# Optimization experiments

Measured on AMD Instinct MI355X. Metric: run time of the kernel, lower is better.

## Reference

```python
import jax, jax.numpy as jnp
import numpy as np

B, T, N, P, L = 8, 96, 20000, 12, 3
D = 32          # d_model (forced by channel-count identity d_model+96 == 4*d_model)
C = 4 * D       # 128 channels inside the linearized conv layers
M = 64          # random_feature_dim
TAU = 0.25
EPS = 1e-6      # numerical_stabilizer in random_feature_map


def _proj_matrix(m, d, seed=0):
    # create_random_matrix: stacked transposed-Q blocks from QR of gaussian blocks,
    # scaled row-wise by norms of a gaussian matrix (scaling=0).
    rng = np.random.RandomState(seed)
    blocks = []
    n_full = m // d
    for _ in range(n_full):
        q, _ = np.linalg.qr(rng.randn(d, d))
        blocks.append(q.T)
    rem = m - n_full * d
    if rem:
        q, _ = np.linalg.qr(rng.randn(d, d))
        blocks.append(q.T[:rem])
    mat = np.vstack(blocks)
    mult = np.linalg.norm(rng.randn(m, d), axis=1)
    return jnp.asarray(mult[:, None] * mat, dtype=jnp.float32)


def setup_inputs() -> dict:
    key = jax.random.key(0)
    ks = jax.random.split(key, 12)
    g = lambda k, shape, s=0.05: jax.random.normal(k, shape, jnp.float32) * s
    return {
        "x": jax.random.normal(ks[0], (B, T, N), jnp.float32),
        "x_mark": jax.random.uniform(ks[1], (B, T, 2), dtype=jnp.float32),
        "node_emb": g(ks[2], (N, D), 0.1),
        "time_tab": g(ks[3], (T, D), 0.1),
        "week_tab": g(ks[4], (7, D), 0.1),
        "input_w": g(ks[5], (D, 3 * T)),
        "input_b": jnp.zeros((D,), jnp.float32),
        "w1_w": g(ks[6], (D, 3 * D)),
        "w1_b": jnp.zeros((D,), jnp.float32),
        "w2_w": g(ks[7], (D, 3 * D)),
        "w2_b": jnp.zeros((D,), jnp.float32),
        "in_w": g(ks[8], (L, C, C)),
        "in_b": jnp.zeros((L, C), jnp.float32),
        "out_w": g(ks[9], (L, C, C)),
        "out_b": jnp.zeros((L, C), jnp.float32),
        "ln_g": jnp.ones((L, C), jnp.float32),
        "ln_b": jnp.zeros((L, C), jnp.float32),
        "reg_w": g(ks[10], (P, 2 * C)),
        "reg_b": jnp.zeros((P,), jnp.float32),
        "proj": _proj_matrix(M, D, seed=0),
    }


def _rfm(data, proj, is_query):
    # FAVOR+ positive random features (head dim == 1 folded out; shapes are [B,N,d])
    d = data.shape[-1]
    data = data * (float(d) ** -0.25)            # h(x) normalizer d^{-1/4}
    ratio = 1.0 / np.sqrt(float(proj.shape[0]))
    dash = jnp.einsum('bnd,md->bnm', data, proj)
    diag = 0.5 * jnp.sum(data * data, axis=-1, keepdims=True)
    if is_query:
        stab = jnp.max(dash, axis=-1, keepdims=True)          # per-row max
    else:
        stab = jnp.max(dash, axis=(1, 2), keepdims=True)      # max over features AND nodes
    return ratio * (jnp.exp(dash - diag - stab) + EPS)


def _linear_kernel(v, phi_q, phi_k):
    # associativity trick: (phi_q (phi_k^T v)) / (phi_q (phi_k^T 1))
    kv = jnp.einsum('bnm,bnc->bmc', phi_k, v)
    num = jnp.einsum('bnm,bmc->bnc', phi_q, kv)
    den = jnp.einsum('bnm,bm->bn', phi_q, jnp.sum(phi_k, axis=1))
    return num / den[..., None]


def reference(x, x_mark, node_emb, time_tab, week_tab, input_w, input_b,
              w1_w, w1_b, w2_w, w2_b, in_w, in_b, out_w, out_b,
              ln_g, ln_b, reg_w, reg_b, proj):
    Bq, Tq, Nq = x.shape
    marks = jax.lax.stop_gradient(x_mark)
    tod_idx = jnp.clip((marks[:, -1, 0] * Tq).astype(jnp.int32), 0, Tq - 1)
    dow_idx = jnp.clip((marks[:, -1, 1] * 7.0).astype(jnp.int32), 0, 6)
    time_e = jnp.broadcast_to(time_tab[tod_idx][:, None, :], (Bq, Nq, D))
    week_e = jnp.broadcast_to(week_tab[dow_idx][:, None, :], (Bq, Nq, D))
    node_e = jnp.broadcast_to(node_emb[None], (Bq, Nq, D))

    # input embedding over the flattened (feature-major) [3*T] channel axis
    tod_f = jnp.broadcast_to(x_mark[:, :, 0:1], (Bq, Tq, Nq))
    dow_f = jnp.broadcast_to(x_mark[:, :, 1:2], (Bq, Tq, Nq))
    feat = jnp.concatenate([x, tod_f, dow_f], axis=1)          # (B, 3T, N)
    x_in = jnp.einsum('bkn,ck->bnc', feat, input_w) + input_b  # (B, N, D)

    xg = jnp.concatenate([node_e, time_e, week_e], axis=-1)        # (B,N,3D)
    h = jnp.concatenate([x_in, node_e, time_e, week_e], axis=-1)   # (B,N,4D)

    inv_sqrt_tau = 1.0 / np.sqrt(TAU)
    nv1 = (jnp.einsum('bng,cg->bnc', xg, w1_w) + w1_b) * inv_sqrt_tau
    nv2 = (jnp.einsum('bng,cg->bnc', xg, w2_w) + w2_b) * inv_sqrt_tau
    # same node vectors (hence same data-derived seed / projection) every layer
    phi_q = _rfm(nv1, proj, True)    # (B,N,M)
    phi_k = _rfm(nv2, proj, False)   # (B,N,M)

    skip = h
    for i in range(L):
        res = h
        u = jax.nn.sigmoid(h @ in_w[i].T + in_b[i]) * (h @ out_w[i].T + out_b[i])
        u = _linear_kernel(u, phi_q, phi_k)
        h = u + res
        mu = jnp.mean(h, axis=-1, keepdims=True)
        var = jnp.var(h, axis=-1, keepdims=True)
        h = (h - mu) * jax.lax.rsqrt(var + 1e-5) * ln_g[i] + ln_b[i]

    out = jnp.concatenate([skip, h], axis=-1) @ reg_w.T + reg_b  # (B,N,P)
    return jnp.swapaxes(out, 1, 2)                               # (B,P,N)
```

## Files before the change

### kernel.cpp

```cpp
#include <hip/hip_runtime.h>

typedef unsigned short u16;
typedef __attribute__((ext_vector_type(8))) __bf16 bf16x8;
typedef __attribute__((ext_vector_type(4))) float f32x4;

#define BB 8
#define TT 96
#define NN 20000
#define NP 20160
#define PP 12
#define LL 3
#define DD 32
#define CC 128
#define MM 64
#define NB3 105
#define NB5 313

constexpr float KSC  = 0.8408964152537145f;
constexpr float KSC2 = 0.7071067811865476f;

__device__ inline u16 f2bf(float f){
  unsigned u = __float_as_uint(f);
  u = (u + 0x7fffu + ((u >> 16) & 1u)) >> 16;
  return (u16)u;
}
__device__ inline float bf2f(u16 h){ return __uint_as_float(((unsigned)h) << 16); }
__device__ inline unsigned fmapu(float f){
  unsigned u = __float_as_uint(f);
  return (u & 0x80000000u) ? ~u : (u | 0x80000000u);
}
__device__ inline float funmap(unsigned u){
  return (u & 0x80000000u) ? __uint_as_float(u & 0x7fffffffu) : __uint_as_float(~u);
}
__device__ inline unsigned pk2(float a, float b){
  return (unsigned)f2bf(a) | ((unsigned)f2bf(b) << 16);
}

__global__ void k0_prep(const float* xm, const float* time_tab, const float* week_tab,
                        const float* w1w, const float* w1b, const float* w2w, const float* w2b,
                        const float* inw, const float* inb, const float* proj,
                        float* bv1, float* bv2, float* sbd1, float* sbd2,
                        float* bc1, float* bc2, float* mb, int* tod, int* dow,
                        unsigned* cmx, float* ksum)
{
  __shared__ float sT[BB][DD], sWk[BB][DD];
  __shared__ float sB1[BB][DD], sB2[BB][DD];
  __shared__ int sTod[BB], sDow[BB];
  int tid = threadIdx.x;
  ksum[tid] = 0.f;
  if (tid < BB){
    float t0 = xm[(tid*TT + TT-1)*2 + 0];
    float t1 = xm[(tid*TT + TT-1)*2 + 1];
    int ti = (int)(t0 * (float)TT); ti = min(max(ti, 0), TT-1);
    int di = (int)(t1 * 7.0f);      di = min(max(di, 0), 6);
    sTod[tid] = ti; sDow[tid] = di; tod[tid] = ti; dow[tid] = di;
  }
  if (tid < MM) cmx[tid] = fmapu(-3e38f);
  __syncthreads();
  if (tid < BB*DD){
    int b = tid >> 5, g = tid & 31;
    sT[b][g]  = time_tab[sTod[b]*DD + g];
    sWk[b][g] = week_tab[sDow[b]*DD + g];
  }
  __syncthreads();
  {
    int which = tid >> 8, b = (tid >> 5) & 7, c = tid & 31;
    const float* w  = which ? w2w : w1w;
    const float* wb = which ? w2b : w1b;
    float s = wb[c];
    for (int g = 0; g < DD; g++)
      s += sT[b][g]*w[c*96 + 32 + g] + sWk[b][g]*w[c*96 + 64 + g];
    if (which){ bv2[b*DD+c] = s; sB2[b][c] = s; }
    else      { bv1[b*DD+c] = s; sB1[b][c] = s; }
  }
  __syncthreads();
  {
    int b = tid >> 6, m = tid & 63;
    float s1 = 0.f, s2 = 0.f;
    for (int c = 0; c < DD; c++){
      float p = proj[m*DD + c];
      s1 += sB1[b][c]*p; s2 += sB2[b][c]*p;
    }
    sbd1[b*MM+m] = KSC * s1;
    sbd2[b*MM+m] = KSC * s2;
  }
  if (tid < 16){
    int b = tid & 7;
    float s = 0.f;
    if (tid >> 3){ for (int c = 0; c < DD; c++) s += sB2[b][c]*sB2[b][c]; bc2[b] = 0.5f*KSC2*s; }
    else         { for (int c = 0; c < DD; c++) s += sB1[b][c]*sB1[b][c]; bc1[b] = 0.5f*KSC2*s; }
  }
  if (tid < 256){
    int b = tid >> 5, c = tid & 31;
    float s = inb[c];
    for (int t = 0; t < TT; t++){
      float m0 = xm[(b*TT+t)*2+0], m1 = xm[(b*TT+t)*2+1];
      s += m0 * inw[c*288 + 96 + t] + m1 * inw[c*288 + 192 + t];
    }
    mb[b*DD+c] = s;
  }
}

__global__ __launch_bounds__(256) void k1_node(
    const float* node_emb, const float* w1w, const float* w2w, const float* proj,
    const float* bv1, const float* bv2,
    const float* gin_w, const float* gout_w,
    float* sd1, float* sd2, float* sq1, float* sq2,
    float* cr1, float* cr2, unsigned* cmx,
    u16* wbf, float* kvz)
{
  __shared__ float sW1[DD][DD], sW2[DD][DD], sP[MM][DD];
  __shared__ float sB1[BB][DD], sB2[BB][DD];
  __shared__ unsigned sCM[MM];
  int tid = threadIdx.x;
  int gid = blockIdx.x*256 + tid;
  for (int i = gid; i < LL*BB*MM*CC; i += 79*256) kvz[i] = 0.f;
  for (int i = gid; i < 2*LL*CC*CC; i += 79*256){
    int which = i / (LL*CC*CC);
    int r = i - which*(LL*CC*CC);
    wbf[i] = f2bf((which ? gout_w : gin_w)[r]);
  }
  for (int i = tid; i < DD*DD; i += 256){
    int c = i >> 5, g = i & 31;
    sW1[c][g] = w1w[c*96 + g];
    sW2[c][g] = w2w[c*96 + g];
  }
  for (int i = tid; i < MM*DD; i += 256) sP[i >> 5][i & 31] = proj[i];
  if (tid < BB*DD){
    int b = tid >> 5, c = tid & 31;
    sB1[b][c] = bv1[tid]; sB2[b][c] = bv2[tid];
  }
  if (tid < MM) sCM[tid] = fmapu(-3e38f);
  __syncthreads();
  int n = blockIdx.x*256 + tid;
  bool valid = n < NN;
  int nc = valid ? n : 0;
  float nd[DD];
  #pragma unroll
  for (int g = 0; g < DD; g += 4){
    float4 v = *(const float4*)&node_emb[nc*DD + g];
    nd[g] = v.x; nd[g+1] = v.y; nd[g+2] = v.z; nd[g+3] = v.w;
  }
  float r1[DD], r2[DD];
  #pragma unroll
  for (int c = 0; c < DD; c++){ r1[c] = 0.f; r2[c] = 0.f; }
  #pragma unroll
  for (int g = 0; g < DD; g++){
    float x = nd[g];
    #pragma unroll
    for (int c = 0; c < DD; c++){ r1[c] += x*sW1[c][g]; r2[c] += x*sW2[c][g]; }
  }
  float q1 = 0.f, q2 = 0.f;
  #pragma unroll
  for (int c = 0; c < DD; c++){ q1 += r1[c]*r1[c]; q2 += r2[c]*r2[c]; }
  if (valid){ sq1[n] = 0.5f*KSC2*q1; sq2[n] = 0.5f*KSC2*q2; }
  for (int b = 0; b < BB; b++){
    float c1 = 0.f, c2 = 0.f;
    #pragma unroll
    for (int c = 0; c < DD; c++){ c1 += r1[c]*sB1[b][c]; c2 += r2[c]*sB2[b][c]; }
    if (valid){ cr1[b*NN + n] = KSC2*c1; cr2[b*NN + n] = KSC2*c2; }
  }
  for (int m = 0; m < MM; m++){
    float s1 = 0.f, s2 = 0.f;
    #pragma unroll
    for (int c = 0; c < DD; c++){ float p = sP[m][c]; s1 += r1[c]*p; s2 += r2[c]*p; }
    s1 *= KSC; s2 *= KSC;
    if (valid){
      sd1[(size_t)n*MM + m] = s1;
      sd2[(size_t)n*MM + m] = s2;
      atomicMax(&sCM[m], fmapu(s2));
    }
  }
  __syncthreads();
  if (tid < MM) atomicMax(&cmx[tid], sCM[tid]);
}

__global__ void k0b_stab(const unsigned* cmx, const float* sbd2, float* stab){
  int lane = threadIdx.x;
  float cm = funmap(cmx[lane]);
  for (int b = 0; b < BB; b++){
    float v = cm + sbd2[b*MM + lane];
    #pragma unroll
    for (int off = 32; off; off >>= 1) v = fmaxf(v, __shfl_xor(v, off));
    if (lane == 0) stab[b] = v;
  }
}

__global__ __launch_bounds__(256) void k1b_phi(
    const float* sd1, const float* sd2, const float* sq1, const float* sq2,
    const float* cr1, const float* cr2, const float* sbd1, const float* sbd2,
    const float* bc1, const float* bc2, const float* stab,
    u16* phiq, u16* phikt, float* ksum)
{
  __shared__ u16 sT[MM][264];
  __shared__ float sQb[MM], sKb[MM];
  __shared__ float sRed[256];
  int tid = threadIdx.x;
  int b = blockIdx.y, n0 = blockIdx.x*256;
  if (tid < MM){
    sQb[tid] = sbd1[b*MM + tid];
    sKb[tid] = sbd2[b*MM + tid] - bc2[b] - stab[b];
  }
  __syncthreads();
  int n = n0 + tid;
  bool v = n < NN;
  int nc = v ? n : 0;
  float dq[MM];
  const float* s1r = sd1 + (size_t)nc*MM;
  #pragma unroll
  for (int m = 0; m < MM; m += 4){
    float4 t = *(const float4*)&s1r[m];
    dq[m]=t.x; dq[m+1]=t.y; dq[m+2]=t.z; dq[m+3]=t.w;
  }
  float rm = -3e38f;
  #pragma unroll
  for (int m = 0; m < MM; m++) rm = fmaxf(rm, dq[m] + sQb[m]);
  float diagq = sq1[nc] + cr1[b*NN + nc] + bc1[b];
  u16* pqr = phiq + ((size_t)(b*NN) + nc)*MM;
  #pragma unroll
  for (int m = 0; m < MM; m += 8){
    float p[8];
    #pragma unroll
    for (int j = 0; j < 8; j++){
      float ev = dq[m+j] + sQb[m+j] - rm - diagq;
      p[j] = 0.125f*__expf(ev) + 1.25e-7f;
    }
    uint4 w = { pk2(p[0],p[1]), pk2(p[2],p[3]), pk2(p[4],p[5]), pk2(p[6],p[7]) };
    if (v) *(uint4*)&pqr[m] = w;
  }
  const float* s2r = sd2 + (size_t)nc*MM;
  float diagk = sq2[nc] + cr2[b*NN + nc];
  #pragma unroll
  for (int m = 0; m < MM; m++){
    float ev = s2r[m] + sKb[m] - diagk;
    float pv = v ? (0.125f*__expf(ev) + 1.25e-7f) : 0.f;
    sT[m][tid] = f2bf(pv);
  }
  __syncthreads();
  {
    int m = tid >> 2, q = tid & 3;
    float s = 0.f;
    for (int j = 0; j < 64; j++) s += bf2f(sT[m][q*64 + j]);
    sRed[tid] = s;
  }
  __syncthreads();
  if (tid < MM){
    float s = sRed[tid*4] + sRed[tid*4+1] + sRed[tid*4+2] + sRed[tid*4+3];
    atomicAdd(&ksum[b*MM + tid], s);
  }
  {
    int m = tid >> 2, q = tid & 3;
    int nb = n0 + q*64;
    if (nb + 64 <= NP){
      u16* dst = phikt + (size_t)(b*MM + m)*NP + nb;
      #pragma unroll
      for (int j = 0; j < 64; j += 8)
        *(uint4*)&dst[j] = *(const uint4*)&sT[m][q*64 + j];
    }
  }
}

__global__ __launch_bounds__(256) void k2_embed(
    const float* x, const float* node_emb, const float* time_tab, const float* week_tab,
    const float* inw, const float* mb, const int* tod, const int* dow,
    u16* skip)
{
  __shared__ float sWt[TT*DD];
  __shared__ float sMB[DD], sTE[DD], sWE[DD];
  int tid = threadIdx.x;
  int b = blockIdx.y;
  for (int i = tid; i < TT*DD; i += 256){
    int t = i >> 5, c = i & 31;
    sWt[i] = inw[c*288 + t];
  }
  if (tid < DD){
    sMB[tid] = mb[b*DD + tid];
    sTE[tid] = time_tab[tod[b]*DD + tid];
    sWE[tid] = week_tab[dow[b]*DD + tid];
  }
  __syncthreads();
  int n = blockIdx.x*256 + tid;
  bool valid = n < NN;
  int nc = valid ? n : 0;
  float acc[DD];
  #pragma unroll
  for (int c = 0; c < DD; c++) acc[c] = sMB[c];
  const float* xb = x + (size_t)b*TT*NN + nc;
  for (int t = 0; t < TT; t++){
    float xv = xb[(size_t)t*NN];
    #pragma unroll
    for (int c = 0; c < DD; c++) acc[c] += xv * sWt[t*DD + c];
  }
  if (!valid) return;
  float nodev[DD];
  #pragma unroll
  for (int g = 0; g < DD; g += 4){
    float4 v = *(const float4*)&node_emb[n*DD + g];
    nodev[g] = v.x; nodev[g+1] = v.y; nodev[g+2] = v.z; nodev[g+3] = v.w;
  }
  auto chv = [&](int c)->float{
    if (c < 32)  return acc[c];
    if (c < 64)  return nodev[c-32];
    if (c < 96)  return sTE[c-64];
    return sWE[c-96];
  };
  u16* dst = skip + (size_t)(b*NN + n)*CC;
  #pragma unroll
  for (int g = 0; g < CC; g += 8){
    uint4 w;
    w.x = pk2(chv(g+0), chv(g+1));
    w.y = pk2(chv(g+2), chv(g+3));
    w.z = pk2(chv(g+4), chv(g+5));
    w.w = pk2(chv(g+6), chv(g+7));
    *(uint4*)&dst[g] = w;
  }
}

__global__ __launch_bounds__(256,2) void k3_gate(
    const u16* hin, const u16* wbf, const float* inb, const float* outb,
    const u16* phikt, float* kv, int layer)
{
  __shared__ u16 sUT[CC*72];
  __shared__ float s_inb[CC], s_outb[CC];
  int tid = threadIdx.x;
  int b = blockIdx.y, blk = blockIdx.x;
  int lane = tid & 63, wave = tid >> 6, quad = lane >> 4, l15 = lane & 15;
  if (tid < CC){ s_inb[tid] = inb[layer*CC + tid]; s_outb[tid] = outb[layer*CC + tid]; }

  bf16x8 bw[4][4];
  #pragma unroll
  for (int nt = 0; nt < 4; nt++){
    int which = nt >> 1;
    int co = wave*32 + (nt & 1)*16 + l15;
    const u16* wp = wbf + ((size_t)(which*LL + layer)*CC + co)*CC;
    #pragma unroll
    for (int ks = 0; ks < 4; ks++)
      bw[ks][nt] = *(const bf16x8*)&wp[ks*32 + quad*8];
  }
  f32x4 kvacc[4][2] = {};
  const u16* hbase = hin + (size_t)(b*NN)*CC;

  for (int ch = 0; ch < 3; ch++){
    int n0 = blk*192 + ch*64;
    f32x4 acc[4][4] = {};
    bf16x8 af[2][4];
    #pragma unroll
    for (int mt = 0; mt < 4; mt++)
      af[0][mt] = *(const bf16x8*)&hbase[(size_t)(n0 + mt*16 + l15)*CC + quad*8];
    #pragma unroll
    for (int ks = 0; ks < 4; ks++){
      int cur = ks & 1, nxt = cur ^ 1;
      if (ks < 3){
        #pragma unroll
        for (int mt = 0; mt < 4; mt++)
          af[nxt][mt] = *(const bf16x8*)&hbase[(size_t)(n0 + mt*16 + l15)*CC + (ks+1)*32 + quad*8];
      }
      #pragma unroll
      for (int mt = 0; mt < 4; mt++)
        #pragma unroll
        for (int nt = 0; nt < 4; nt++)
          acc[mt][nt] = __builtin_amdgcn_mfma_f32_16x16x32_bf16(af[cur][mt], bw[ks][nt], acc[mt][nt], 0, 0, 0);
    }
    __syncthreads();
    #pragma unroll
    for (int mt = 0; mt < 4; mt++){
      int r0 = mt*16 + quad*4;
      #pragma unroll
      for (int nt = 0; nt < 2; nt++){
        int co = wave*32 + nt*16 + l15;
        float bi = s_inb[co], bo = s_outb[co];
        float uv[4];
        #pragma unroll
        for (int e = 0; e < 4; e++){
          float up = acc[mt][nt][e] + bi;
          float vp = acc[mt][nt+2][e] + bo;
          float u = vp / (1.f + __expf(-up));
          if (n0 + r0 + e >= NN) u = 0.f;
          uv[e] = u;
        }
        ushort4 hv4;
        hv4.x = f2bf(uv[0]); hv4.y = f2bf(uv[1]); hv4.z = f2bf(uv[2]); hv4.w = f2bf(uv[3]);
        *(ushort4*)&sUT[co*72 + r0] = hv4;
      }
    }
    __syncthreads();
    #pragma unroll
    for (int ks2 = 0; ks2 < 2; ks2++){
      bf16x8 ap[4], bu[2];
      #pragma unroll
      for (int mtp = 0; mtp < 4; mtp++)
        ap[mtp] = *(const bf16x8*)&phikt[(size_t)(b*MM + mtp*16 + l15)*NP + n0 + ks2*32 + quad*8];
      #pragma unroll
      for (int nt2 = 0; nt2 < 2; nt2++)
        bu[nt2] = *(const bf16x8*)&sUT[(wave*32 + nt2*16 + l15)*72 + ks2*32 + quad*8];
      #pragma unroll
      for (int mtp = 0; mtp < 4; mtp++)
        #pragma unroll
        for (int nt2 = 0; nt2 < 2; nt2++)
          kvacc[mtp][nt2] = __builtin_amdgcn_mfma_f32_16x16x32_bf16(ap[mtp], bu[nt2], kvacc[mtp][nt2], 0, 0, 0);
    }
  }
  float* kvb = kv + (size_t)(layer*BB + b)*MM*CC;
  #pragma unroll
  for (int mt = 0; mt < 4; mt++)
    #pragma unroll
    for (int nt2 = 0; nt2 < 2; nt2++)
      #pragma unroll
      for (int e = 0; e < 4; e++)
        atomicAdd(&kvb[(mt*16 + quad*4 + e)*CC + wave*32 + nt2*16 + l15], kvacc[mt][nt2][e]);
}

__global__ void k4_reduce(const float* kv, const float* ksum, u16* kvt, int layer){
  int b = blockIdx.x;
  int tid = threadIdx.x;
  const float* kvb = kv + (size_t)(layer*BB + b)*MM*CC;
  for (int idx = tid; idx < 144*MM; idx += 256){
    int c = idx >> 6, m = idx & 63;
    float v = (c < CC) ? kvb[m*CC + c] : ((c == CC) ? ksum[b*MM + m] : 0.f);
    kvt[(size_t)b*144*MM + idx] = f2bf(v);
  }
}

__global__ __launch_bounds__(256) void k5_attn(
    const u16* hin, u16* hout, const u16* phiq, const u16* kvt,
    const float* lng, const float* lnb, int layer)
{
  __shared__ u16 sH[64*132];
  __shared__ u16 sKv[144*72];
  __shared__ float sLg[CC], sLb[CC];
  int tid = threadIdx.x;
  int b = blockIdx.y, n0 = blockIdx.x*64;
  int lane = tid & 63, wave = tid >> 6, quad = lane >> 4, l15 = lane & 15;
  for (int idx = tid; idx < 144*8; idx += 256){
    int c = idx >> 3, g = idx & 7;
    *(uint4*)&sKv[c*72 + g*8] = *(const uint4*)&kvt[(size_t)b*144*MM + c*MM + g*8];
  }
  if (tid < CC){ sLg[tid] = lng[layer*CC + tid]; sLb[tid] = lnb[layer*CC + tid]; }
  {
    int r = tid >> 2, seg = tid & 3;
    int n = n0 + r;
    const u16* src = hin + (size_t)(b*NN + min(n, NN-1))*CC + seg*32;
    #pragma unroll
    for (int k = 0; k < 32; k += 8){
      uint4 d = *(const uint4*)&src[k];
      *(uint2*)&sH[r*132 + seg*32 + k]     = make_uint2(d.x, d.y);
      *(uint2*)&sH[r*132 + seg*32 + k + 4] = make_uint2(d.z, d.w);
    }
  }
  __syncthreads();
  bf16x8 aq[2];
  #pragma unroll
  for (int ks = 0; ks < 2; ks++)
    aq[ks] = *(const bf16x8*)&phiq[((size_t)(b*NN) + n0 + wave*16 + l15)*MM + ks*32 + quad*8];
  f32x4 nacc[9] = {};
  #pragma unroll
  for (int ks = 0; ks < 2; ks++)
    #pragma unroll
    for (int nt = 0; nt < 9; nt++){
      bf16x8 bk = *(const bf16x8*)&sKv[(nt*16 + l15)*72 + ks*32 + quad*8];
      nacc[nt] = __builtin_amdgcn_mfma_f32_16x16x32_bf16(aq[ks], bk, nacc[nt], 0, 0, 0);
    }
  #pragma unroll
  for (int e = 0; e < 4; e++){
    float den = __shfl(nacc[8][e], lane & 48);
    int rml = wave*16 + quad*4 + e;
    float y[8];
    float s1 = 0.f, s2 = 0.f;
    #pragma unroll
    for (int nt = 0; nt < 8; nt++){
      float res = bf2f(sH[rml*132 + nt*16 + l15]);
      float yv = nacc[nt][e]/den + res;
      y[nt] = yv; s1 += yv; s2 += yv*yv;
    }
    #pragma unroll
    for (int off = 1; off < 16; off <<= 1){
      s1 += __shfl_xor(s1, off);
      s2 += __shfl_xor(s2, off);
    }
    float mu = s1 * (1.f/CC);
    float rs = rsqrtf(s2 * (1.f/CC) - mu*mu + 1e-5f);
    #pragma unroll
    for (int nt = 0; nt < 8; nt++){
      int c = nt*16 + l15;
      sH[rml*132 + c] = f2bf((y[nt] - mu)*rs*sLg[c] + sLb[c]);
    }
  }
  __syncthreads();
  {
    int r = tid >> 2, seg = tid & 3;
    int n = n0 + r;
    if (n < NN){
      u16* dst = hout + (size_t)(b*NN + n)*CC + seg*32;
      #pragma unroll
      for (int k = 0; k < 32; k += 8){
        uint2 a = *(const uint2*)&sH[r*132 + seg*32 + k];
        uint2 c2 = *(const uint2*)&sH[r*132 + seg*32 + k + 4];
        uint4 w = { a.x, a.y, c2.x, c2.y };
        *(uint4*)&dst[k] = w;
      }
    }
  }
}

__global__ __launch_bounds__(256) void k6_final(
    const u16* skip, const u16* hbuf, const float* regw, const float* regb,
    float* out)
{
  __shared__ float sRW[PP*256];
  __shared__ float sRB[PP];
  int tid = threadIdx.x;
  for (int i = tid; i < PP*256; i += 256) sRW[i] = regw[i];
  if (tid < PP) sRB[tid] = regb[tid];
  __syncthreads();
  int b = blockIdx.y;
  int n = blockIdx.x*256 + tid;
  if (n >= NN) return;
  float acc[PP];
  #pragma unroll
  for (int p = 0; p < PP; p++) acc[p] = sRB[p];
  const u16* sr = skip + (size_t)(b*NN + n)*CC;
  const u16* hr = hbuf + (size_t)(b*NN + n)*CC;
  for (int half = 0; half < 2; half++){
    const u16* src = half ? hr : sr;
    int coff = half*128;
    for (int k = 0; k < CC; k += 8){
      uint4 d = *(const uint4*)&src[k];
      float v0 = __uint_as_float(d.x<<16), v1 = __uint_as_float(d.x & 0xffff0000u);
      float v2 = __uint_as_float(d.y<<16), v3 = __uint_as_float(d.y & 0xffff0000u);
      float v4 = __uint_as_float(d.z<<16), v5 = __uint_as_float(d.z & 0xffff0000u);
      float v6 = __uint_as_float(d.w<<16), v7 = __uint_as_float(d.w & 0xffff0000u);
      #pragma unroll
      for (int p = 0; p < PP; p++){
        const float* wr = &sRW[p*256 + coff + k];
        acc[p] += v0*wr[0] + v1*wr[1] + v2*wr[2] + v3*wr[3]
                + v4*wr[4] + v5*wr[5] + v6*wr[6] + v7*wr[7];
      }
    }
  }
  #pragma unroll
  for (int p = 0; p < PP; p++)
    out[(size_t)(b*PP + p)*NN + n] = acc[p];
}

extern "C" void kernel_launch(void* const* d_in, const int* in_sizes, int n_in,
                              void* d_out, int out_size, void* d_ws, size_t ws_size,
                              hipStream_t stream)
{
  const float* x        = (const float*)d_in[0];
  const float* xm       = (const float*)d_in[1];
  const float* node_emb = (const float*)d_in[2];
  const float* time_tab = (const float*)d_in[3];
  const float* week_tab = (const float*)d_in[4];
  const float* input_w  = (const float*)d_in[5];
  const float* input_b  = (const float*)d_in[6];
  const float* w1w      = (const float*)d_in[7];
  const float* w1b      = (const float*)d_in[8];
  const float* w2w      = (const float*)d_in[9];
  const float* w2b      = (const float*)d_in[10];
  const float* inw      = (const float*)d_in[11];
  const float* inb      = (const float*)d_in[12];
  const float* outw     = (const float*)d_in[13];
  const float* outb     = (const float*)d_in[14];
  const float* lng      = (const float*)d_in[15];
  const float* lnb      = (const float*)d_in[16];
  const float* regw     = (const float*)d_in[17];
  const float* regb     = (const float*)d_in[18];
  const float* proj     = (const float*)d_in[19];
  float* out = (float*)d_out;

  char* wsb = (char*)d_ws;
  size_t off = 0;
  auto alloc = [&](size_t bytes)->char*{
    char* p = wsb + off; off += (bytes + 255) & ~(size_t)255; return p;
  };
  u16*   skip  = (u16*)  alloc((size_t)BB*NN*CC*2);
  u16*   hbuf  = (u16*)  alloc((size_t)BB*NN*CC*2);
  u16*   phiq  = (u16*)  alloc((size_t)BB*NN*MM*2);
  u16*   phikt = (u16*)  alloc((size_t)BB*MM*NP*2 + 4096);
  float* sd1   = (float*)alloc((size_t)NN*MM*4);
  float* sd2   = (float*)alloc((size_t)NN*MM*4);
  float* sq1   = (float*)alloc((size_t)NN*4);
  float* sq2   = (float*)alloc((size_t)NN*4);
  float* cr1   = (float*)alloc((size_t)BB*NN*4);
  float* cr2   = (float*)alloc((size_t)BB*NN*4);
  u16*   wbf   = (u16*)  alloc((size_t)2*LL*CC*CC*2);
  float* kv    = (float*)alloc((size_t)LL*BB*MM*CC*4);
  u16*   kvt   = (u16*)  alloc((size_t)BB*144*MM*2);
  float* ksum  = (float*)alloc(BB*MM*4);
  float* bv1   = (float*)alloc(BB*DD*4);
  float* bv2   = (float*)alloc(BB*DD*4);
  float* sbd1  = (float*)alloc(BB*MM*4);
  float* sbd2  = (float*)alloc(BB*MM*4);
  float* bc1   = (float*)alloc(BB*4);
  float* bc2   = (float*)alloc(BB*4);
  float* mb    = (float*)alloc(BB*DD*4);
  int*   tod   = (int*)  alloc(BB*4);
  int*   dow   = (int*)  alloc(BB*4);
  unsigned* cmx= (unsigned*)alloc(MM*4);
  float* stab  = (float*)alloc(BB*4);
  (void)ws_size; (void)in_sizes; (void)n_in; (void)out_size;

  k0_prep<<<1, 512, 0, stream>>>(xm, time_tab, week_tab, w1w, w1b, w2w, w2b,
                                 input_w, input_b, proj,
                                 bv1, bv2, sbd1, sbd2, bc1, bc2, mb, tod, dow, cmx, ksum);
  k1_node<<<79, 256, 0, stream>>>(node_emb, w1w, w2w, proj, bv1, bv2, inw, outw,
                                  sd1, sd2, sq1, sq2, cr1, cr2, cmx, wbf, kv);
  k0b_stab<<<1, 64, 0, stream>>>(cmx, sbd2, stab);
  k1b_phi<<<dim3(79, 8), 256, 0, stream>>>(sd1, sd2, sq1, sq2, cr1, cr2,
                                           sbd1, sbd2, bc1, bc2, stab,
                                           phiq, phikt, ksum);
  k2_embed<<<dim3(79, 8), 256, 0, stream>>>(x, node_emb, time_tab, week_tab,
                                            input_w, mb, tod, dow, skip);
  for (int l = 0; l < LL; l++){
    const u16* hi = (l == 0) ? skip : hbuf;
    k3_gate<<<dim3(NB3, 8), 256, 0, stream>>>(hi, wbf, inb, outb, phikt, kv, l);
    k4_reduce<<<8, 256, 0, stream>>>(kv, ksum, kvt, l);
    k5_attn<<<dim3(NB5, 8), 256, 0, stream>>>(hi, hbuf, phiq, kvt, lng, lnb, l);
  }
  k6_final<<<dim3(79, 8), 256, 0, stream>>>(skip, hbuf, regw, regb, out);
}
```

Baseline: 803.1 us.

## Precompose node-vector and projection weights; split node kernel four threads per node

The prep kernel now precomputes W·proj and W·bias products, so the node kernel maps node embeddings straight to random-feature logits and cross terms without first forming the 32-dim intermediate. The node kernel is re-partitioned so four threads share each node (313 blocks instead of 79). Each thread writes its slice with float4 stores and the per-node squared norm is combined by shuffles. The aim is fewer FLOPs, less register pressure and better GPU occupancy in a kernel that previously launched only 79 blocks, at the cost of extra work in the single-block prep kernel.

Measured after the change: 661.1 us. 1.21x faster.

```diff
diff --git a/kernel.cpp b/kernel.cpp
--- a/kernel.cpp
+++ b/kernel.cpp
@@ -15,6 +15,7 @@
 #define MM 64
 #define NB3 105
 #define NB5 313
+#define NB1 313
 
 constexpr float KSC  = 0.8408964152537145f;
 constexpr float KSC2 = 0.7071067811865476f;
@@ -41,13 +42,20 @@
                         const float* inw, const float* inb, const float* proj,
                         float* bv1, float* bv2, float* sbd1, float* sbd2,
                         float* bc1, float* bc2, float* mb, int* tod, int* dow,
-                        unsigned* cmx, float* ksum)
+                        unsigned* cmx, float* ksum, float* qmat, float* emat)
 {
   __shared__ float sT[BB][DD], sWk[BB][DD];
   __shared__ float sB1[BB][DD], sB2[BB][DD];
+  __shared__ float sW1G[DD][DD], sW2G[DD][DD], sPJ[MM][DD];
   __shared__ int sTod[BB], sDow[BB];
   int tid = threadIdx.x;
   ksum[tid] = 0.f;
+  for (int i = tid; i < DD*DD; i += 512){
+    int c = i >> 5, g = i & 31;
+    sW1G[c][g] = w1w[c*96 + g];
+    sW2G[c][g] = w2w[c*96 + g];
+  }
+  for (int i = tid; i < MM*DD; i += 512) sPJ[i >> 5][i & 31] = proj[i];
   if (tid < BB){
     float t0 = xm[(tid*TT + TT-1)*2 + 0];
     float t1 = xm[(tid*TT + TT-1)*2 + 1];
@@ -74,11 +82,25 @@
     else      { bv1[b*DD+c] = s; sB1[b][c] = s; }
   }
   __syncthreads();
+  for (int e = tid; e < 2*DD*MM; e += 512){
+    int set = e >> 11, g = (e >> 6) & 31, m = e & 63;
+    float s = 0.f;
+    if (set == 0){ for (int c = 0; c < DD; c++) s += sW1G[c][g]*sPJ[m][c]; }
+    else         { for (int c = 0; c < DD; c++) s += sW2G[c][g]*sPJ[m][c]; }
+    qmat[e] = KSC * s;
+  }
+  {
+    int set = tid >> 8, g = (tid >> 3) & 31, b = tid & 7;
+    float s = 0.f;
+    if (set == 0){ for (int c = 0; c < DD; c++) s += sW1G[c][g]*sB1[b][c]; }
+    else         { for (int c = 0; c < DD; c++) s += sW2G[c][g]*sB2[b][c]; }
+    emat[tid] = KSC2 * s;
+  }
   {
     int b = tid >> 6, m = tid & 63;
     float s1 = 0.f, s2 = 0.f;
     for (int c = 0; c < DD; c++){
-      float p = proj[m*DD + c];
+      float p = sPJ[m][c];
       s1 += sB1[b][c]*p; s2 += sB2[b][c]*p;
     }
     sbd1[b*MM+m] = KSC * s1;
@@ -102,37 +124,36 @@
 }
 
 __global__ __launch_bounds__(256) void k1_node(
-    const float* node_emb, const float* w1w, const float* w2w, const float* proj,
-    const float* bv1, const float* bv2,
+    const float* node_emb, const float* w1w, const float* w2w,
+    const float* qmat, const float* emat,
     const float* gin_w, const float* gout_w,
     float* sd1, float* sd2, float* sq1, float* sq2,
     float* cr1, float* cr2, unsigned* cmx,
     u16* wbf, float* kvz)
 {
-  __shared__ float sW1[DD][DD], sW2[DD][DD], sP[MM][DD];
-  __shared__ float sB1[BB][DD], sB2[BB][DD];
+  __shared__ float sQ1[DD*MM], sQ2[DD*MM];
+  __shared__ float sW1[DD*DD], sW2[DD*DD];
+  __shared__ float sE[2*DD*BB];
   __shared__ unsigned sCM[MM];
   int tid = threadIdx.x;
   int gid = blockIdx.x*256 + tid;
-  for (int i = gid; i < LL*BB*MM*CC; i += 79*256) kvz[i] = 0.f;
-  for (int i = gid; i < 2*LL*CC*CC; i += 79*256){
+  const int TOT = NB1*256;
+  for (int i = gid; i < LL*BB*MM*CC; i += TOT) kvz[i] = 0.f;
+  for (int i = gid; i < 2*LL*CC*CC; i += TOT){
     int which = i / (LL*CC*CC);
     int r = i - which*(LL*CC*CC);
     wbf[i] = f2bf((which ? gout_w : gin_w)[r]);
   }
+  for (int i = tid; i < DD*MM; i += 256){ sQ1[i] = qmat[i]; sQ2[i] = qmat[DD*MM + i]; }
   for (int i = tid; i < DD*DD; i += 256){
-    int c = i >> 5, g = i & 31;
-    sW1[c][g] = w1w[c*96 + g];
-    sW2[c][g] = w2w[c*96 + g];
-  }
-  for (int i = tid; i < MM*DD; i += 256) sP[i >> 5][i & 31] = proj[i];
-  if (tid < BB*DD){
-    int b = tid >> 5, c = tid & 31;
-    sB1[b][c] = bv1[tid]; sB2[b][c] = bv2[tid];
-  }
+    sW1[i] = w1w[(i>>5)*96 + (i&31)];
+    sW2[i] = w2w[(i>>5)*96 + (i&31)];
+  }
+  for (int i = tid; i < 2*DD*BB; i += 256) sE[i] = emat[i];
   if (tid < MM) sCM[tid] = fmapu(-3e38f);
   __syncthreads();
-  int n = blockIdx.x*256 + tid;
+  int r = tid >> 2, q = tid & 3;
+  int n = blockIdx.x*64 + r;
   bool valid = n < NN;
   int nc = valid ? n : 0;
   float nd[DD];
@@ -141,34 +162,65 @@
     float4 v = *(const float4*)&node_emb[nc*DD + g];
     nd[g] = v.x; nd[g+1] = v.y; nd[g+2] = v.z; nd[g+3] = v.w;
   }
-  float r1[DD], r2[DD];
-  #pragma unroll
-  for (int c = 0; c < DD; c++){ r1[c] = 0.f; r2[c] = 0.f; }
+  float s1v[16], s2v[16];
+  #pragma unroll
+  for (int j = 0; j < 16; j++){ s1v[j] = 0.f; s2v[j] = 0.f; }
   #pragma unroll
   for (int g = 0; g < DD; g++){
-    float x = nd[g];
-    #pragma unroll
-    for (int c = 0; c < DD; c++){ r1[c] += x*sW1[c][g]; r2[c] += x*sW2[c][g]; }
-  }
-  float q1 = 0.f, q2 = 0.f;
-  #pragma unroll
-  for (int c = 0; c < DD; c++){ q1 += r1[c]*r1[c]; q2 += r2[c]*r2[c]; }
-  if (valid){ sq1[n] = 0.5f*KSC2*q1; sq2[n] = 0.5f*KSC2*q2; }
-  for (int b = 0; b < BB; b++){
-    float c1 = 0.f, c2 = 0.f;
-    #pragma unroll
-    for (int c = 0; c < DD; c++){ c1 += r1[c]*sB1[b][c]; c2 += r2[c]*sB2[b][c]; }
-    if (valid){ cr1[b*NN + n] = KSC2*c1; cr2[b*NN + n] = KSC2*c2; }
-  }
-  for (int m = 0; m < MM; m++){
-    float s1 = 0.f, s2 = 0.f;
-    #pragma unroll
-    for (int c = 0; c < DD; c++){ float p = sP[m][c]; s1 += r1[c]*p; s2 += r2[c]*p; }
-    s1 *= KSC; s2 *= KSC;
+    float xg = nd[g];
+    #pragma unroll
+    for (int jj = 0; jj < 16; jj += 4){
+      float4 a1 = *(const float4*)&sQ1[g*MM + q*16 + jj];
+      float4 a2 = *(const float4*)&sQ2[g*MM + q*16 + jj];
+      s1v[jj+0] += xg*a1.x; s1v[jj+1] += xg*a1.y; s1v[jj+2] += xg*a1.z; s1v[jj+3] += xg*a1.w;
+      s2v[jj+0] += xg*a2.x; s2v[jj+1] += xg*a2.y; s2v[jj+2] += xg*a2.z; s2v[jj+3] += xg*a2.w;
+    }
+  }
+  if (valid){
+    #pragma unroll
+    for (int jj = 0; jj < 16; jj += 4){
+      *(float4*)&sd1[(size_t)n*MM + q*16 + jj] = make_float4(s1v[jj], s1v[jj+1], s1v[jj+2], s1v[jj+3]);
+      *(float4*)&sd2[(size_t)n*MM + q*16 + jj] = make_float4(s2v[jj], s2v[jj+1], s2v[jj+2], s2v[jj+3]);
+    }
+    #pragma unroll
+    for (int j = 0; j < 16; j++)
+      atomicMax(&sCM[q*16 + j], fmapu(s2v[j]));
+  }
+  float sqp1 = 0.f, sqp2 = 0.f;
+  #pragma unroll
+  for (int c8 = 0; c8 < 8; c8++){
+    int c = q*8 + c8;
+    float d1 = 0.f, d2 = 0.f;
+    #pragma unroll
+    for (int g = 0; g < DD; g += 4){
+      float4 w1v = *(const float4*)&sW1[c*DD + g];
+      float4 w2v = *(const float4*)&sW2[c*DD + g];
+      d1 += nd[g]*w1v.x + nd[g+1]*w1v.y + nd[g+2]*w1v.z + nd[g+3]*w1v.w;
+      d2 += nd[g]*w2v.x + nd[g+1]*w2v.y + nd[g+2]*w2v.z + nd[g+3]*w2v.w;
+    }
+    sqp1 += d1*d1; sqp2 += d2*d2;
+  }
+  sqp1 += __shfl_xor(sqp1, 1); sqp1 += __shfl_xor(sqp1, 2);
+  sqp2 += __shfl_xor(sqp2, 1); sqp2 += __shfl_xor(sqp2, 2);
+  if (q == 0 && valid){
+    sq1[n] = 0.5f*KSC2*sqp1;
+    sq2[n] = 0.5f*KSC2*sqp2;
+  }
+  {
+    float cA1 = 0.f, cB1 = 0.f, cA2 = 0.f, cB2 = 0.f;
+    #pragma unroll
+    for (int g = 0; g < DD; g++){
+      float xg = nd[g];
+      cA1 += xg*sE[g*8 + 2*q];
+      cB1 += xg*sE[g*8 + 2*q + 1];
+      cA2 += xg*sE[256 + g*8 + 2*q];
+      cB2 += xg*sE[256 + g*8 + 2*q + 1];
+    }
     if (valid){
-      sd1[(size_t)n*MM + m] = s1;
-      sd2[(size_t)n*MM + m] = s2;
-      atomicMax(&sCM[m], fmapu(s2));
+      cr1[(2*q)*NN + n]     = cA1;
+      cr1[(2*q+1)*NN + n]   = cB1;
+      cr2[(2*q)*NN + n]     = cA2;
+      cr2[(2*q+1)*NN + n]   = cB2;
     }
   }
   __syncthreads();
@@ -598,13 +650,16 @@
   int*   dow   = (int*)  alloc(BB*4);
   unsigned* cmx= (unsigned*)alloc(MM*4);
   float* stab  = (float*)alloc(BB*4);
+  float* qmat  = (float*)alloc(2*DD*MM*4);
+  float* emat  = (float*)alloc(2*DD*BB*4);
   (void)ws_size; (void)in_sizes; (void)n_in; (void)out_size;
 
   k0_prep<<<1, 512, 0, stream>>>(xm, time_tab, week_tab, w1w, w1b, w2w, w2b,
                                  input_w, input_b, proj,
-                                 bv1, bv2, sbd1, sbd2, bc1, bc2, mb, tod, dow, cmx, ksum);
-  k1_node<<<79, 256, 0, stream>>>(node_emb, w1w, w2w, proj, bv1, bv2, inw, outw,
-                                  sd1, sd2, sq1, sq2, cr1, cr2, cmx, wbf, kv);
+                                 bv1, bv2, sbd1, sbd2, bc1, bc2, mb, tod, dow, cmx, ksum,
+                                 qmat, emat);
+  k1_node<<<NB1, 256, 0, stream>>>(node_emb, w1w, w2w, qmat, emat, inw, outw,
+                                   sd1, sd2, sq1, sq2, cr1, cr2, cmx, wbf, kv);
   k0b_stab<<<1, 64, 0, stream>>>(cmx, sbd2, stab);
   k1b_phi<<<dim3(79, 8), 256, 0, stream>>>(sd1, sd2, sq1, sq2, cr1, cr2,
                                            sbd1, sbd2, bc1, bc2, stab,
```
